# Performance work log

Hardware: AMD Instinct MI355X
Metric: run time of the kernel (lower is better)

Reference implementation:

```python
import jax, jax.numpy as jnp
import numpy as np

NUM_NODES = 50000
NUM_HYPEREDGES = 10000
NUM_INCIDENCES = 800000
CHANNELS = 256
NEG_SLOPE = 0.01  # torch leaky_relu default negative_slope


def setup_inputs() -> dict:
    key = jax.random.key(0)
    k_n, k_e, k_emb, k_cw, k_lw, k_lb = jax.random.split(key, 6)
    node_idx = jax.random.randint(k_n, (NUM_INCIDENCES,), 0, NUM_NODES, dtype=jnp.int32)
    edge_idx = jax.random.randint(k_e, (NUM_INCIDENCES,), 0, NUM_HYPEREDGES, dtype=jnp.int32)
    edge_index = jnp.stack([node_idx, edge_idx], axis=0)  # [2, nnz] incidence list
    s = 1.0 / np.sqrt(CHANNELS).astype(np.float32)
    emb = jax.random.normal(k_emb, (NUM_NODES, CHANNELS), jnp.float32)  # Node2Vec embedding table
    conv_w = jax.random.normal(k_cw, (CHANNELS, CHANNELS), jnp.float32) * s  # HypergraphConv.lin (no bias)
    conv_b = jnp.zeros((CHANNELS,), jnp.float32)  # HypergraphConv.bias
    lin_w = jax.random.normal(k_lw, (CHANNELS, CHANNELS), jnp.float32) * s
    lin_b = jax.random.normal(k_lb, (CHANNELS,), jnp.float32) * s
    return {"emb": emb, "conv_w": conv_w, "conv_b": conv_b,
            "lin_w": lin_w, "lin_b": lin_b, "edge_index": edge_index}


def reference(emb, conv_w, conv_b, lin_w, lin_b, edge_index):
    node_idx, edge_idx = edge_index[0], edge_index[1]
    # HypergraphConv (use_attention=False): X' = D^-1 H B^-1 H^T (X W^T) + b
    x = emb @ conv_w.T  # [N, C]
    ones = jnp.ones((NUM_INCIDENCES,), x.dtype)
    D = jax.ops.segment_sum(ones, node_idx, num_segments=NUM_NODES)       # node degree
    Dinv = jnp.where(D > 0, 1.0 / D, 0.0)
    B = jax.ops.segment_sum(ones, edge_idx, num_segments=NUM_HYPEREDGES)  # hyperedge degree
    Binv = jnp.where(B > 0, 1.0 / B, 0.0)
    # node -> hyperedge aggregation
    e = jax.ops.segment_sum(x[node_idx], edge_idx, num_segments=NUM_HYPEREDGES) * Binv[:, None]  # [E, C]
    # hyperedge -> node aggregation
    n = jax.ops.segment_sum(e[edge_idx], node_idx, num_segments=NUM_NODES) * Dinv[:, None] + conv_b  # [N, C]
    y = jax.nn.leaky_relu(n, NEG_SLOPE)
    g = y.T @ y  # [C, C] Gram
    out = jax.nn.leaky_relu(g @ lin_w.T + lin_b, NEG_SLOPE)
    return out
```

## Files before the change

### kernel.cpp

```cpp
#include <hip/hip_runtime.h>

#define N_NODES 50000
#define N_EDGES 10000
#define NNZ     800000
#define C       256
#define SLOPE   0.01f
#define KTOT    50176
#define KCHUNK  512
#define NZB     98
#define MPAD    10048

#define NB      250
#define EB_E    40
#define EB_N    200
#define CHUNK   3125
#define CAP     6000

#define OFF_CC_E    0
#define OFF_CC_N    1024
#define OFF_CUR_E   2048
#define OFF_CUR_N   3072
#define ZERO_BYTES  4096
#define OFF_G       4096
#define OFF_CB_E    266240
#define OFF_CB_N    267264
#define OFF_RS_N    268288
#define OFF_RS_E    468480
#define OFF_BUF_E   508672
#define OFF_BUF_N   3708672
#define OFF_CSR_E   6908672
#define OFF_CSR_N   10108672
#define OFF_EMBH    13308672
#define OFF_YT      13308672
#define OFF_EACC    39000064
#define OFF_E2      44144640
#define OFF_CWH     49289216
#define OFF_PART    49420288

typedef __attribute__((ext_vector_type(8))) short short8;
typedef __attribute__((ext_vector_type(4))) float floatx4;

static __device__ __forceinline__ unsigned short f2bf(float f) {
    unsigned int u = __float_as_uint(f);
    u = (u + 0x7fffu + ((u >> 16) & 1u)) >> 16;
    return (unsigned short)u;
}

static __device__ __forceinline__ void acc_bf8(const uint4 d, float* a) {
    a[0] += __uint_as_float(d.x << 16);
    a[1] += __uint_as_float(d.x & 0xffff0000u);
    a[2] += __uint_as_float(d.y << 16);
    a[3] += __uint_as_float(d.y & 0xffff0000u);
    a[4] += __uint_as_float(d.z << 16);
    a[5] += __uint_as_float(d.z & 0xffff0000u);
    a[6] += __uint_as_float(d.w << 16);
    a[7] += __uint_as_float(d.w & 0xffff0000u);
}

static __device__ __forceinline__ void gather4(const uint4* __restrict__ tbl4,
                                               const int* __restrict__ csr,
                                               int s, int t, int half, int l32,
                                               int zrow, float* a) {
    for (int i = s + half; i < t; i += 8) {
        int e0 = csr[i];
        int e1 = (i + 2 < t) ? csr[i + 2] : zrow;
        int e2 = (i + 4 < t) ? csr[i + 4] : zrow;
        int e3 = (i + 6 < t) ? csr[i + 6] : zrow;
        uint4 d0 = tbl4[(size_t)e0 * 32 + l32];
        uint4 d1 = tbl4[(size_t)e1 * 32 + l32];
        uint4 d2 = tbl4[(size_t)e2 * 32 + l32];
        uint4 d3 = tbl4[(size_t)e3 * 32 + l32];
        acc_bf8(d0, a); acc_bf8(d1, a); acc_bf8(d2, a); acc_bf8(d3, a);
    }
}

static __device__ __forceinline__ void gather8(const uint4* __restrict__ tbl4,
                                               const int* __restrict__ csr,
                                               int s, int t, int half, int l32,
                                               int zrow, float* a) {
    for (int i = s + half; i < t; i += 16) {
        int e0 = csr[i];
        int e1 = (i + 2  < t) ? csr[i + 2]  : zrow;
        int e2 = (i + 4  < t) ? csr[i + 4]  : zrow;
        int e3 = (i + 6  < t) ? csr[i + 6]  : zrow;
        int e4 = (i + 8  < t) ? csr[i + 8]  : zrow;
        int e5 = (i + 10 < t) ? csr[i + 10] : zrow;
        int e6 = (i + 12 < t) ? csr[i + 12] : zrow;
        int e7 = (i + 14 < t) ? csr[i + 14] : zrow;
        uint4 d0 = tbl4[(size_t)e0 * 32 + l32];
        uint4 d1 = tbl4[(size_t)e1 * 32 + l32];
        uint4 d2 = tbl4[(size_t)e2 * 32 + l32];
        uint4 d3 = tbl4[(size_t)e3 * 32 + l32];
        uint4 d4 = tbl4[(size_t)e4 * 32 + l32];
        uint4 d5 = tbl4[(size_t)e5 * 32 + l32];
        uint4 d6 = tbl4[(size_t)e6 * 32 + l32];
        uint4 d7 = tbl4[(size_t)e7 * 32 + l32];
        acc_bf8(d0, a); acc_bf8(d1, a); acc_bf8(d2, a); acc_bf8(d3, a);
        acc_bf8(d4, a); acc_bf8(d5, a); acc_bf8(d6, a); acc_bf8(d7, a);
    }
}

__global__ __launch_bounds__(256) void zero_kernel(float4* __restrict__ p, int n4) {
    int i = blockIdx.x * 256 + threadIdx.x;
    if (i < n4) p[i] = make_float4(0.f, 0.f, 0.f, 0.f);
}

__global__ __launch_bounds__(256) void cast_bf16_kernel(const float4* __restrict__ src4,
                                                        uint4* __restrict__ dst4,
                                                        int src_n8, int n8) {
    int i = blockIdx.x * 256 + threadIdx.x;
    if (i >= n8) return;
    uint4 o = {0u, 0u, 0u, 0u};
    if (i < src_n8) {
        float4 f0 = src4[2 * i], f1 = src4[2 * i + 1];
        o.x = f2bf(f0.x) | ((unsigned)f2bf(f0.y) << 16);
        o.y = f2bf(f0.z) | ((unsigned)f2bf(f0.w) << 16);
        o.z = f2bf(f1.x) | ((unsigned)f2bf(f1.y) << 16);
        o.w = f2bf(f1.z) | ((unsigned)f2bf(f1.w) << 16);
    }
    dst4[i] = o;
}

__global__ __launch_bounds__(256) void coarse_count_kernel(const int* __restrict__ node_idx,
                                                           const int* __restrict__ edge_idx,
                                                           int* __restrict__ cc_e,
                                                           int* __restrict__ cc_n) {
    __shared__ int he[NB], hn[NB];
    int tid = threadIdx.x;
    int base = blockIdx.x * CHUNK;
    for (int i = tid; i < NB; i += 256) { he[i] = 0; hn[i] = 0; }
    __syncthreads();
    for (int i = tid; i < CHUNK; i += 256) {
        atomicAdd(&he[edge_idx[base + i] / EB_E], 1);
        atomicAdd(&hn[node_idx[base + i] / EB_N], 1);
    }
    __syncthreads();
    for (int k = tid; k < NB; k += 256) {
        if (he[k]) atomicAdd(&cc_e[k], he[k]);
        if (hn[k]) atomicAdd(&cc_n[k], hn[k]);
    }
}

__global__ __launch_bounds__(256) void coarse_scan_kernel(const int* __restrict__ cc_e,
                                                          const int* __restrict__ cc_n,
                                                          int* __restrict__ cb_e,
                                                          int* __restrict__ cb_n) {
    __shared__ int tmp[256];
    int tid = threadIdx.x;
    int v = (tid < NB) ? cc_e[tid] : 0;
    tmp[tid] = v;
    __syncthreads();
    for (int off = 1; off < 256; off <<= 1) {
        int t = (tid >= off) ? tmp[tid - off] : 0;
        __syncthreads();
        tmp[tid] += t;
        __syncthreads();
    }
    if (tid < NB) cb_e[tid + 1] = tmp[tid];
    if (tid == 0) cb_e[0] = 0;
    __syncthreads();
    v = (tid < NB) ? cc_n[tid] : 0;
    tmp[tid] = v;
    __syncthreads();
    for (int off = 1; off < 256; off <<= 1) {
        int t = (tid >= off) ? tmp[tid - off] : 0;
        __syncthreads();
        tmp[tid] += t;
        __syncthreads();
    }
    if (tid < NB) cb_n[tid + 1] = tmp[tid];
    if (tid == 0) cb_n[0] = 0;
}

__global__ __launch_bounds__(256) void bucket_scatter_kernel(const int* __restrict__ node_idx,
                                                             const int* __restrict__ edge_idx,
                                                             const int* __restrict__ cb_e,
                                                             const int* __restrict__ cb_n,
                                                             int* __restrict__ cur_e,
                                                             int* __restrict__ cur_n,
                                                             int* __restrict__ buf_e,
                                                             int* __restrict__ buf_n) {
    __shared__ int he[NB], hn[NB], be[NB], bn[NB];
    int tid = threadIdx.x;
    int base = blockIdx.x * CHUNK;
    for (int i = tid; i < NB; i += 256) { he[i] = 0; hn[i] = 0; }
    __syncthreads();
    for (int i = tid; i < CHUNK; i += 256) {
        int e = edge_idx[base + i], v = node_idx[base + i];
        atomicAdd(&he[e / EB_E], 1);
        atomicAdd(&hn[v / EB_N], 1);
    }
    __syncthreads();
    for (int k = tid; k < NB; k += 256) {
        int c = he[k];
        be[k] = cb_e[k] + (c ? atomicAdd(&cur_e[k], c) : 0);
        int cn = hn[k];
        bn[k] = cb_n[k] + (cn ? atomicAdd(&cur_n[k], cn) : 0);
    }
    __syncthreads();
    for (int i = tid; i < NB; i += 256) { he[i] = 0; hn[i] = 0; }
    __syncthreads();
    for (int i = tid; i < CHUNK; i += 256) {
        int e = edge_idx[base + i], v = node_idx[base + i];
        int ke = e / EB_E, kn = v / EB_N;
        int oe = atomicAdd(&he[ke], 1);
        buf_e[be[ke] + oe] = (v << 6) | (e - ke * EB_E);
        int on = atomicAdd(&hn[kn], 1);
        buf_n[bn[kn] + on] = (e << 8) | (v - kn * EB_N);
    }
}

__global__ __launch_bounds__(256) void bucket_sort_kernel(const int* __restrict__ buf_e,
                                                          const int* __restrict__ buf_n,
                                                          const int* __restrict__ cb_e,
                                                          const int* __restrict__ cb_n,
                                                          int* __restrict__ csr_e,
                                                          int* __restrict__ csr_n,
                                                          int* __restrict__ rs_e,
                                                          int* __restrict__ rs_n) {
    __shared__ int A[CAP];
    __shared__ int h[EB_N], bs[EB_N];
    int tid = threadIdx.x;
    bool edgeSide = blockIdx.x < NB;
    int k = edgeSide ? blockIdx.x : blockIdx.x - NB;
    int eb = edgeSide ? EB_E : EB_N;
    int shift = edgeSide ? 6 : 8;
    int mask = (1 << shift) - 1;
    const int* cb  = edgeSide ? cb_e : cb_n;
    const int* buf = edgeSide ? buf_e : buf_n;
    int* csr       = edgeSide ? csr_e : csr_n;
    int* rs        = edgeSide ? rs_e : rs_n;
    int base = cb[k];
    int cnt = cb[k + 1] - base;
    for (int i = tid; i < eb; i += 256) h[i] = 0;
    __syncthreads();
    for (int i = tid; i < cnt; i += 256) {
        int it = buf[base + i];
        if (i < CAP) A[i] = it;
        atomicAdd(&h[it & mask], 1);
    }
    __syncthreads();
    if (tid == 0) {
        int s = 0;
        for (int j = 0; j < eb; j++) { bs[j] = s; s += h[j]; }
    }
    __syncthreads();
    for (int j = tid; j < eb; j += 256) {
        rs[k * eb + j] = base + bs[j];
        h[j] = 0;
    }
    if (tid == 0 && k == NB - 1) rs[edgeSide ? N_EDGES : N_NODES] = NNZ;
    __syncthreads();
    for (int i = tid; i < cnt; i += 256) {
        int it = (i < CAP) ? A[i] : buf[base + i];
        int loc = it & mask;
        int off = bs[loc] + atomicAdd(&h[loc], 1);
        csr[base + off] = it >> shift;
    }
}

__global__ __launch_bounds__(256) void edge_aggregate_kernel(const uint4* __restrict__ embh4,
                                                             const int* __restrict__ csr_e,
                                                             const int* __restrict__ rs_e,
                                                             unsigned short* __restrict__ e_acc_h) {
    int e = blockIdx.x * 4 + (threadIdx.x >> 6);
    int lane = threadIdx.x & 63;
    int half = lane >> 5, l32 = lane & 31;
    int s = 0, t = 0;
    if (e < N_EDGES) { s = rs_e[e]; t = rs_e[e + 1]; }
    float a[8] = {0.f, 0.f, 0.f, 0.f, 0.f, 0.f, 0.f, 0.f};
    gather8(embh4, csr_e, s, t, half, l32, N_NODES, a);
    #pragma unroll
    for (int j = 0; j < 8; j++) a[j] += __shfl_xor(a[j], 32);
    if (half == 0) {
        uint4 o;
        o.x = f2bf(a[0]) | ((unsigned)f2bf(a[1]) << 16);
        o.y = f2bf(a[2]) | ((unsigned)f2bf(a[3]) << 16);
        o.z = f2bf(a[4]) | ((unsigned)f2bf(a[5]) << 16);
        o.w = f2bf(a[6]) | ((unsigned)f2bf(a[7]) << 16);
        ((uint4*)(e_acc_h + (size_t)e * C))[l32] = o;
    }
}

__global__ __launch_bounds__(256) void edge_gemm_mfma_kernel(const unsigned short* __restrict__ e_acc_h,
                                                             const unsigned short* __restrict__ cwh,
                                                             const int* __restrict__ rs_e,
                                                             unsigned short* __restrict__ e2h) {
    __shared__ __align__(16) unsigned short As[64 * 72];
    __shared__ __align__(16) unsigned short Bs[64 * 72];
    int i0 = blockIdx.x * 64, j0 = blockIdx.y * 64;
    int tid = threadIdx.x;
    int w = tid >> 6, lane = tid & 63;
    int col = lane & 15, quad = lane >> 4;
    floatx4 acc[4] = {};
    for (int step = 0; step < 4; step++) {
        int kb = step * 64;
        __syncthreads();
        #pragma unroll
        for (int l = 0; l < 2; l++) {
            int slot = tid + l * 256;
            int row = slot >> 3, grp = slot & 7;
            uint4 da = *(const uint4*)(e_acc_h + (size_t)(i0 + row) * C + kb + grp * 8);
            *(uint4*)(&As[row * 72 + grp * 8]) = da;
            uint4 db = *(const uint4*)(cwh + (size_t)(j0 + row) * C + kb + grp * 8);
            *(uint4*)(&Bs[row * 72 + grp * 8]) = db;
        }
        __syncthreads();
        #pragma unroll
        for (int sub = 0; sub < 2; sub++) {
            short8 a = *(const short8*)(&As[(w * 16 + col) * 72 + sub * 32 + quad * 8]);
            #pragma unroll
            for (int jt = 0; jt < 4; jt++) {
                short8 b = *(const short8*)(&Bs[(jt * 16 + col) * 72 + sub * 32 + quad * 8]);
                acc[jt] = __builtin_amdgcn_mfma_f32_16x16x32_bf16(a, b, acc[jt], 0, 0, 0);
            }
        }
    }
    #pragma unroll
    for (int r = 0; r < 4; r++) {
        int m = i0 + w * 16 + quad * 4 + r;
        int deg = (m < N_EDGES) ? rs_e[m + 1] - rs_e[m] : 0;
        float binv = (deg > 0) ? 1.0f / (float)deg : 0.0f;
        #pragma unroll
        for (int jt = 0; jt < 4; jt++)
            e2h[(size_t)m * C + j0 + jt * 16 + col] = f2bf(acc[jt][r] * binv);
    }
}

__global__ __launch_bounds__(256) void node_aggregate_t_kernel(const uint4* __restrict__ e2h4,
                                                               const int* __restrict__ csr_n,
                                                               const int* __restrict__ rs_n,
                                                               const float* __restrict__ conv_b,
                                                               unsigned short* __restrict__ yT) {
    __shared__ __align__(16) unsigned short T[32][256];
    int n0 = blockIdx.x * 32;
    int tid = threadIdx.x;
    int w = tid >> 6, lane = tid & 63;
    int half = lane >> 5, l32 = lane & 31;
    int base = n0 + w * 8;
    int rsv = rs_n[min(base + lane, N_NODES)];
    float4 b0 = ((const float4*)conv_b)[l32 * 2];
    float4 b1 = ((const float4*)conv_b)[l32 * 2 + 1];
    float bb[8] = {b0.x, b0.y, b0.z, b0.w, b1.x, b1.y, b1.z, b1.w};
    for (int q = 0; q < 8; q++) {
        int v = base + q;
        int s = __shfl(rsv, q), t = __shfl(rsv, q + 1);
        float a[8] = {0.f, 0.f, 0.f, 0.f, 0.f, 0.f, 0.f, 0.f};
        gather4(e2h4, csr_n, s, t, half, l32, N_EDGES, a);
        #pragma unroll
        for (int j = 0; j < 8; j++) a[j] += __shfl_xor(a[j], 32);
        float dinv = (t > s) ? 1.0f / (float)(t - s) : 0.0f;
        unsigned int pk[4];
        #pragma unroll
        for (int j = 0; j < 4; j++) {
            float r0 = a[2 * j] * dinv + bb[2 * j];
            float r1 = a[2 * j + 1] * dinv + bb[2 * j + 1];
            r0 = (r0 > 0.f) ? r0 : SLOPE * r0;
            r1 = (r1 > 0.f) ? r1 : SLOPE * r1;
            if (v >= N_NODES) { r0 = 0.f; r1 = 0.f; }
            pk[j] = f2bf(r0) | ((unsigned)f2bf(r1) << 16);
        }
        if (half == 0) {
            uint4 o; o.x = pk[0]; o.y = pk[1]; o.z = pk[2]; o.w = pk[3];
            *(uint4*)(&T[w * 8 + q][l32 * 8]) = o;
        }
    }
    __syncthreads();
    int ch = tid;
    #pragma unroll
    for (int jj = 0; jj < 4; jj++) {
        uint4 o;
        o.x = T[jj * 8 + 0][ch] | ((unsigned)T[jj * 8 + 1][ch] << 16);
        o.y = T[jj * 8 + 2][ch] | ((unsigned)T[jj * 8 + 3][ch] << 16);
        o.z = T[jj * 8 + 4][ch] | ((unsigned)T[jj * 8 + 5][ch] << 16);
        o.w = T[jj * 8 + 6][ch] | ((unsigned)T[jj * 8 + 7][ch] << 16);
        *(uint4*)(yT + (size_t)ch * KTOT + n0 + jj * 8) = o;
    }
}

__global__ __launch_bounds__(256) void gram_mfma_kernel(const unsigned short* __restrict__ yT,
                                                        float* __restrict__ part) {
    static const int PI[10] = {0, 0, 0, 0, 1, 1, 1, 2, 2, 3};
    static const int PJ[10] = {0, 1, 2, 3, 1, 2, 3, 2, 3, 3};
    __shared__ __align__(16) unsigned short As[64 * 72];
    __shared__ __align__(16) unsigned short Bs[64 * 72];
    int i0 = PI[blockIdx.x] * 64, j0 = PJ[blockIdx.x] * 64;
    bool diag = (i0 == j0);
    int kb0 = blockIdx.y * KCHUNK;
    int tid = threadIdx.x;
    int w = tid >> 6, lane = tid & 63;
    int col = lane & 15, quad = lane >> 4;
    floatx4 acc[4] = {};
    for (int step = 0; step < KCHUNK / 64; step++) {
        int kb = kb0 + step * 64;
        __syncthreads();
        #pragma unroll
        for (int l = 0; l < 2; l++) {
            int slot = tid + l * 256;
            int row = slot >> 3, grp = slot & 7;
            uint4 da = *(const uint4*)(yT + (size_t)(i0 + row) * KTOT + kb + grp * 8);
            *(uint4*)(&As[row * 72 + grp * 8]) = da;
            if (!diag) {
                uint4 db = *(const uint4*)(yT + (size_t)(j0 + row) * KTOT + kb + grp * 8);
                *(uint4*)(&Bs[row * 72 + grp * 8]) = db;
            }
        }
        __syncthreads();
        const unsigned short* Bb = diag ? As : Bs;
        #pragma unroll
        for (int sub = 0; sub < 2; sub++) {
            short8 a = *(const short8*)(&As[(w * 16 + col) * 72 + sub * 32 + quad * 8]);
            #pragma unroll
            for (int jt = 0; jt < 4; jt++) {
                short8 b = *(const short8*)(&Bb[(jt * 16 + col) * 72 + sub * 32 + quad * 8]);
                acc[jt] = __builtin_amdgcn_mfma_f32_16x16x32_bf16(a, b, acc[jt], 0, 0, 0);
            }
        }
    }
    float* slab = part + ((size_t)blockIdx.y * 10 + blockIdx.x) * 4096;
    #pragma unroll
    for (int jt = 0; jt < 4; jt++)
        #pragma unroll
        for (int r = 0; r < 4; r++)
            slab[(w * 16 + quad * 4 + r) * 64 + jt * 16 + col] = acc[jt][r];
}

__global__ __launch_bounds__(256) void greduce_kernel(const float* __restrict__ part,
                                                      float* __restrict__ g) {
    int i = blockIdx.x, j = threadIdx.x;
    int a = i >> 6, b = j >> 6;
    int lo = min(a, b), hi = max(a, b);
    int t = lo * (7 - lo) / 2 + hi;
    int li = (a <= b) ? (i & 63) : (j & 63);
    int lj = (a <= b) ? (j & 63) : (i & 63);
    const float* p = part + (size_t)t * 4096 + li * 64 + lj;
    float s = 0.f;
    for (int z = 0; z < NZB; z++) s += p[(size_t)z * 40960];
    g[(size_t)i * C + j] = s;
}

__global__ __launch_bounds__(256) void out_kernel(const float* __restrict__ g,
                                                  const float* __restrict__ lin_w,
                                                  const float* __restrict__ lin_b,
                                                  float* __restrict__ out) {
    __shared__ float gs[C];
    int i = blockIdx.x, j = threadIdx.x;
    gs[j] = g[(size_t)i * C + j];
    __syncthreads();
    float acc = lin_b[j];
    const float* wrow = lin_w + (size_t)j * C;
    for (int k = 0; k < C; k++) acc += gs[k] * wrow[k];
    out[(size_t)i * C + j] = (acc > 0.f) ? acc : SLOPE * acc;
}

extern "C" void kernel_launch(void* const* d_in, const int* in_sizes, int n_in,
                              void* d_out, int out_size, void* d_ws, size_t ws_size,
                              hipStream_t stream) {
    const float* emb    = (const float*)d_in[0];
    const float* conv_w = (const float*)d_in[1];
    const float* conv_b = (const float*)d_in[2];
    const float* lin_w  = (const float*)d_in[3];
    const float* lin_b  = (const float*)d_in[4];
    const int*   eidx   = (const int*)d_in[5];
    const int* node_idx = eidx;
    const int* edge_idx = eidx + NNZ;

    char* ws = (char*)d_ws;
    int* cc_e  = (int*)(ws + OFF_CC_E);
    int* cc_n  = (int*)(ws + OFF_CC_N);
    int* cur_e = (int*)(ws + OFF_CUR_E);
    int* cur_n = (int*)(ws + OFF_CUR_N);
    float* g   = (float*)(ws + OFF_G);
    int* cb_e  = (int*)(ws + OFF_CB_E);
    int* cb_n  = (int*)(ws + OFF_CB_N);
    int* rs_n  = (int*)(ws + OFF_RS_N);
    int* rs_e  = (int*)(ws + OFF_RS_E);
    int* buf_e = (int*)(ws + OFF_BUF_E);
    int* buf_n = (int*)(ws + OFF_BUF_N);
    int* csr_e = (int*)(ws + OFF_CSR_E);
    int* csr_n = (int*)(ws + OFF_CSR_N);
    uint4* embh4 = (uint4*)(ws + OFF_EMBH);
    unsigned short* e_acc_h = (unsigned short*)(ws + OFF_EACC);
    unsigned short* e2h = (unsigned short*)(ws + OFF_E2);
    unsigned short* cwh = (unsigned short*)(ws + OFF_CWH);
    unsigned short* yT  = (unsigned short*)(ws + OFF_YT);
    float* part = (float*)(ws + OFF_PART);
    float* out = (float*)d_out;

    int n4 = ZERO_BYTES / 16;
    zero_kernel<<<1, 256, 0, stream>>>((float4*)ws, n4);

    cast_bf16_kernel<<<6251, 256, 0, stream>>>((const float4*)emb, embh4, 1600000, 1600032);
    cast_bf16_kernel<<<32, 256, 0, stream>>>((const float4*)conv_w, (uint4*)cwh, 8192, 8192);

    coarse_count_kernel<<<256, 256, 0, stream>>>(node_idx, edge_idx, cc_e, cc_n);

    coarse_scan_kernel<<<1, 256, 0, stream>>>(cc_e, cc_n, cb_e, cb_n);

    bucket_scatter_kernel<<<256, 256, 0, stream>>>(node_idx, edge_idx, cb_e, cb_n,
                                                   cur_e, cur_n, buf_e, buf_n);

    bucket_sort_kernel<<<2 * NB, 256, 0, stream>>>(buf_e, buf_n, cb_e, cb_n,
                                                   csr_e, csr_n, rs_e, rs_n);

    edge_aggregate_kernel<<<MPAD / 4, 256, 0, stream>>>(embh4, csr_e, rs_e, e_acc_h);

    edge_gemm_mfma_kernel<<<dim3(MPAD / 64, C / 64), 256, 0, stream>>>(e_acc_h, cwh, rs_e, e2h);

    node_aggregate_t_kernel<<<KTOT / 32, 256, 0, stream>>>((const uint4*)e2h, csr_n, rs_n,
                                                           conv_b, yT);

    gram_mfma_kernel<<<dim3(10, NZB), 256, 0, stream>>>(yT, part);

    greduce_kernel<<<C, 256, 0, stream>>>(part, g);

    out_kernel<<<C, 256, 0, stream>>>(g, lin_w, lin_b, out);
}
```

Measured before the change: 307.1 us.

## Fuse prep kernels, reuse local atomic offsets in scatter, merge reduce with output

Merges the two bf16 cast launches and the coarse count into one heterogeneous prep kernel, so the independent work runs concurrently and fewer launches are needed. The bucket scatter keeps the per-element shared-atomic offsets from its first pass in registers, which removes the second histogram pass and its atomics. The Gram partial reduction is fused with the final linear layer, so the intermediate g buffer is never written and read back. The cost is more register pressure in the scatter kernel, and a prep kernel whose blocks have uneven amounts of work.

New measurement: 301.1 us, median of 2. Within noise of the previous version (-2.0%).

```diff
diff --git a/kernel.cpp b/kernel.cpp
--- a/kernel.cpp
+++ b/kernel.cpp
@@ -21,7 +21,6 @@
 #define OFF_CUR_E   2048
 #define OFF_CUR_N   3072
 #define ZERO_BYTES  4096
-#define OFF_G       4096
 #define OFF_CB_E    266240
 #define OFF_CB_N    267264
 #define OFF_RS_N    268288
@@ -105,39 +104,52 @@
     if (i < n4) p[i] = make_float4(0.f, 0.f, 0.f, 0.f);
 }
 
-__global__ __launch_bounds__(256) void cast_bf16_kernel(const float4* __restrict__ src4,
-                                                        uint4* __restrict__ dst4,
-                                                        int src_n8, int n8) {
-    int i = blockIdx.x * 256 + threadIdx.x;
-    if (i >= n8) return;
-    uint4 o = {0u, 0u, 0u, 0u};
-    if (i < src_n8) {
-        float4 f0 = src4[2 * i], f1 = src4[2 * i + 1];
+#define PREP_EMB_BLOCKS 6251
+#define PREP_CW_BLOCKS  32
+__global__ __launch_bounds__(256) void prep_kernel(const float4* __restrict__ emb4,
+                                                   uint4* __restrict__ embh4,
+                                                   const float4* __restrict__ cw4,
+                                                   uint4* __restrict__ cwh4,
+                                                   const int* __restrict__ node_idx,
+                                                   const int* __restrict__ edge_idx,
+                                                   int* __restrict__ cc_e,
+                                                   int* __restrict__ cc_n) {
+    __shared__ int he[NB], hn[NB];
+    int b = blockIdx.x, tid = threadIdx.x;
+    if (b < PREP_EMB_BLOCKS) {
+        int i = b * 256 + tid;
+        if (i >= 1600032) return;
+        uint4 o = {0u, 0u, 0u, 0u};
+        if (i < 1600000) {
+            float4 f0 = emb4[2 * i], f1 = emb4[2 * i + 1];
+            o.x = f2bf(f0.x) | ((unsigned)f2bf(f0.y) << 16);
+            o.y = f2bf(f0.z) | ((unsigned)f2bf(f0.w) << 16);
+            o.z = f2bf(f1.x) | ((unsigned)f2bf(f1.y) << 16);
+            o.w = f2bf(f1.z) | ((unsigned)f2bf(f1.w) << 16);
+        }
+        embh4[i] = o;
+    } else if (b < PREP_EMB_BLOCKS + PREP_CW_BLOCKS) {
+        int i = (b - PREP_EMB_BLOCKS) * 256 + tid;
+        float4 f0 = cw4[2 * i], f1 = cw4[2 * i + 1];
+        uint4 o;
         o.x = f2bf(f0.x) | ((unsigned)f2bf(f0.y) << 16);
         o.y = f2bf(f0.z) | ((unsigned)f2bf(f0.w) << 16);
         o.z = f2bf(f1.x) | ((unsigned)f2bf(f1.y) << 16);
         o.w = f2bf(f1.z) | ((unsigned)f2bf(f1.w) << 16);
-    }
-    dst4[i] = o;
-}
-
-__global__ __launch_bounds__(256) void coarse_count_kernel(const int* __restrict__ node_idx,
-                                                           const int* __restrict__ edge_idx,
-                                                           int* __restrict__ cc_e,
-                                                           int* __restrict__ cc_n) {
-    __shared__ int he[NB], hn[NB];
-    int tid = threadIdx.x;
-    int base = blockIdx.x * CHUNK;
-    for (int i = tid; i < NB; i += 256) { he[i] = 0; hn[i] = 0; }
-    __syncthreads();
-    for (int i = tid; i < CHUNK; i += 256) {
-        atomicAdd(&he[edge_idx[base + i] / EB_E], 1);
-        atomicAdd(&hn[node_idx[base + i] / EB_N], 1);
-    }
-    __syncthreads();
-    for (int k = tid; k < NB; k += 256) {
-        if (he[k]) atomicAdd(&cc_e[k], he[k]);
-        if (hn[k]) atomicAdd(&cc_n[k], hn[k]);
+        cwh4[i] = o;
+    } else {
+        int base = (b - PREP_EMB_BLOCKS - PREP_CW_BLOCKS) * CHUNK;
+        for (int i = tid; i < NB; i += 256) { he[i] = 0; hn[i] = 0; }
+        __syncthreads();
+        for (int i = tid; i < CHUNK; i += 256) {
+            atomicAdd(&he[edge_idx[base + i] / EB_E], 1);
+            atomicAdd(&hn[node_idx[base + i] / EB_N], 1);
+        }
+        __syncthreads();
+        for (int k = tid; k < NB; k += 256) {
+            if (he[k]) atomicAdd(&cc_e[k], he[k]);
+            if (hn[k]) atomicAdd(&cc_n[k], hn[k]);
+        }
     }
 }
 
@@ -185,10 +197,16 @@
     int base = blockIdx.x * CHUNK;
     for (int i = tid; i < NB; i += 256) { he[i] = 0; hn[i] = 0; }
     __syncthreads();
-    for (int i = tid; i < CHUNK; i += 256) {
-        int e = edge_idx[base + i], v = node_idx[base + i];
-        atomicAdd(&he[e / EB_E], 1);
-        atomicAdd(&hn[v / EB_N], 1);
+    int pe[13], pn[13];
+    #pragma unroll
+    for (int k = 0; k < 13; k++) {
+        int i = tid + k * 256;
+        if (i < CHUNK) {
+            int e = edge_idx[base + i], v = node_idx[base + i];
+            int ke = e / EB_E, kn = v / EB_N;
+            pe[k] = (ke << 12) | atomicAdd(&he[ke], 1);
+            pn[k] = (kn << 12) | atomicAdd(&hn[kn], 1);
+        }
     }
     __syncthreads();
     for (int k = tid; k < NB; k += 256) {
@@ -198,15 +216,16 @@
         bn[k] = cb_n[k] + (cn ? atomicAdd(&cur_n[k], cn) : 0);
     }
     __syncthreads();
-    for (int i = tid; i < NB; i += 256) { he[i] = 0; hn[i] = 0; }
-    __syncthreads();
-    for (int i = tid; i < CHUNK; i += 256) {
-        int e = edge_idx[base + i], v = node_idx[base + i];
-        int ke = e / EB_E, kn = v / EB_N;
-        int oe = atomicAdd(&he[ke], 1);
-        buf_e[be[ke] + oe] = (v << 6) | (e - ke * EB_E);
-        int on = atomicAdd(&hn[kn], 1);
-        buf_n[bn[kn] + on] = (e << 8) | (v - kn * EB_N);
+    #pragma unroll
+    for (int k = 0; k < 13; k++) {
+        int i = tid + k * 256;
+        if (i < CHUNK) {
+            int e = edge_idx[base + i], v = node_idx[base + i];
+            int ke = pe[k] >> 12, oe = pe[k] & 4095;
+            buf_e[be[ke] + oe] = (v << 6) | (e - ke * EB_E);
+            int kn = pn[k] >> 12, on = pn[k] & 4095;
+            buf_n[bn[kn] + on] = (e << 8) | (v - kn * EB_N);
+        }
     }
 }
 
@@ -425,8 +444,11 @@
             slab[(w * 16 + quad * 4 + r) * 64 + jt * 16 + col] = acc[jt][r];
 }
 
-__global__ __launch_bounds__(256) void greduce_kernel(const float* __restrict__ part,
-                                                      float* __restrict__ g) {
+__global__ __launch_bounds__(256) void greduce_out_kernel(const float* __restrict__ part,
+                                                          const float* __restrict__ lin_w,
+                                                          const float* __restrict__ lin_b,
+                                                          float* __restrict__ out) {
+    __shared__ float gs[C];
     int i = blockIdx.x, j = threadIdx.x;
     int a = i >> 6, b = j >> 6;
     int lo = min(a, b), hi = max(a, b);
@@ -436,16 +458,7 @@
     const float* p = part + (size_t)t * 4096 + li * 64 + lj;
     float s = 0.f;
     for (int z = 0; z < NZB; z++) s += p[(size_t)z * 40960];
-    g[(size_t)i * C + j] = s;
-}
-
-__global__ __launch_bounds__(256) void out_kernel(const float* __restrict__ g,
-                                                  const float* __restrict__ lin_w,
-                                                  const float* __restrict__ lin_b,
-                                                  float* __restrict__ out) {
-    __shared__ float gs[C];
-    int i = blockIdx.x, j = threadIdx.x;
-    gs[j] = g[(size_t)i * C + j];
+    gs[j] = s;
     __syncthreads();
     float acc = lin_b[j];
     const float* wrow = lin_w + (size_t)j * C;
@@ -470,7 +483,6 @@
     int* cc_n  = (int*)(ws + OFF_CC_N);
     int* cur_e = (int*)(ws + OFF_CUR_E);
     int* cur_n = (int*)(ws + OFF_CUR_N);
-    float* g   = (float*)(ws + OFF_G);
     int* cb_e  = (int*)(ws + OFF_CB_E);
     int* cb_n  = (int*)(ws + OFF_CB_N);
     int* rs_n  = (int*)(ws + OFF_RS_N);
@@ -487,13 +499,11 @@
     float* part = (float*)(ws + OFF_PART);
     float* out = (float*)d_out;
 
-    int n4 = ZERO_BYTES / 16;
-    zero_kernel<<<1, 256, 0, stream>>>((float4*)ws, n4);
-
-    cast_bf16_kernel<<<6251, 256, 0, stream>>>((const float4*)emb, embh4, 1600000, 1600032);
-    cast_bf16_kernel<<<32, 256, 0, stream>>>((const float4*)conv_w, (uint4*)cwh, 8192, 8192);
-
-    coarse_count_kernel<<<256, 256, 0, stream>>>(node_idx, edge_idx, cc_e, cc_n);
+    zero_kernel<<<1, 256, 0, stream>>>((float4*)ws, ZERO_BYTES / 16);
+
+    prep_kernel<<<PREP_EMB_BLOCKS + PREP_CW_BLOCKS + 256, 256, 0, stream>>>(
+        (const float4*)emb, embh4, (const float4*)conv_w, (uint4*)cwh,
+        node_idx, edge_idx, cc_e, cc_n);
 
     coarse_scan_kernel<<<1, 256, 0, stream>>>(cc_e, cc_n, cb_e, cb_n);
 
@@ -512,7 +522,5 @@
 
     gram_mfma_kernel<<<dim3(10, NZB), 256, 0, stream>>>(yT, part);
 
-    greduce_kernel<<<C, 256, 0, stream>>>(part, g);
-
-    out_kernel<<<C, 256, 0, stream>>>(g, lin_w, lin_b, out);
-}
+    greduce_out_kernel<<<C, 256, 0, stream>>>(part, lin_w, lin_b, out);
+}
```
